# Kernel optimization log

Measured on AMD Instinct MI355X. Metric: run time of the kernel, lower is better.

The kernel has to match this reference:

```python
import jax, jax.numpy as jnp
import numpy as np

K = 1024          # codebook size
D = 64            # embedding dim
CC = 0.25         # commitment cost


def setup_inputs() -> dict:
    key = jax.random.key(0)
    k1, k2 = jax.random.split(key)
    inputs = jax.random.normal(k1, (64, 64, 32, 32), dtype=jnp.float32)  # [B, C=D, H, W]
    # nn.Embedding weight init: uniform(-1/K, 1/K)
    embedding = jax.random.uniform(k2, (K, D), dtype=jnp.float32,
                                   minval=-1.0 / K, maxval=1.0 / K)
    return {"inputs": inputs, "embedding": embedding}


def reference(inputs, embedding):
    # NCHW -> NHWC
    x = jnp.transpose(inputs, (0, 2, 3, 1))            # [B, H, W, D]
    B, H, W, Dd = x.shape
    flat = x.reshape(-1, Dd)                           # [N, D]
    distances = (jnp.sum(flat * flat, axis=1, keepdims=True)
                 - 2.0 * flat @ embedding.T
                 + jnp.sum(embedding * embedding, axis=1)[None, :])
    encoding_indices = jnp.argmin(distances, axis=1)   # [N]
    encodings = encoding_indices.reshape(B, H, W)      # [B, H, W]
    quantized = embedding[encodings]                   # [B, H, W, D]

    e_latent_loss = jnp.mean((jax.lax.stop_gradient(quantized) - x) ** 2)
    q_latent_loss = jnp.mean((quantized - jax.lax.stop_gradient(x)) ** 2)
    loss = q_latent_loss + CC * e_latent_loss

    # straight-through estimator
    quantized_st = x + jax.lax.stop_gradient(quantized - x)
    out = jnp.transpose(quantized_st, (0, 3, 1, 2))    # NHWC -> NCHW
    nll = jnp.ones((1,), dtype=jnp.float32)
    return out, encodings, loss, nll
```

## Files before the change

### kernel.cpp

```cpp
#include <hip/hip_runtime.h>
#include <stdint.h>

constexpr int KCODES = 1024;
constexpr int DDIM   = 64;
constexpr int HW     = 1024;
constexpr int NPTS   = 65536;
constexpr int PPB    = 64;
constexpr int NBLK   = NPTS / PPB;

constexpr int OUT_Q    = 0;
constexpr int OUT_IDX  = 4194304;
constexpr int OUT_LOSS = 4259840;
constexpr int OUT_NLL  = 4259841;

constexpr int WS_MAXC  = 0;
constexpr int WS_C     = 16;
constexpr int WS_E     = 2048;
constexpr int WS_PART  = 34816;

typedef __attribute__((ext_vector_type(8))) short short8v;
typedef __attribute__((ext_vector_type(4))) float float4v;

__device__ __forceinline__ uint16_t f2bf(float f) {
    uint32_t u = __float_as_uint(f);
    return (uint16_t)((u + 0x7fffu + ((u >> 16) & 1u)) >> 16);
}
__device__ __forceinline__ uint32_t pack2bf(float a, float b) {
    return (uint32_t)f2bf(a) | ((uint32_t)f2bf(b) << 16);
}

__device__ __forceinline__ float np_pairwise_sumsq64(const float* a) {
    float r[8];
    #pragma unroll
    for (int j = 0; j < 8; ++j) r[j] = __fmul_rn(a[j], a[j]);
    #pragma unroll
    for (int i = 8; i < 64; i += 8)
        #pragma unroll
        for (int j = 0; j < 8; ++j)
            r[j] = __fadd_rn(r[j], __fmul_rn(a[i + j], a[i + j]));
    return __fadd_rn(__fadd_rn(__fadd_rn(r[0], r[1]), __fadd_rn(r[2], r[3])),
                     __fadd_rn(__fadd_rn(r[4], r[5]), __fadd_rn(r[6], r[7])));
}

__global__ __launch_bounds__(256) void vq_init(const float* __restrict__ emb,
                                               float* __restrict__ ws) {
    __shared__ float smax[4];
    const int k = blockIdx.x * 256 + threadIdx.x;
    float row[DDIM];
    const float4* src = (const float4*)(emb + (size_t)k * DDIM);
    #pragma unroll
    for (int j = 0; j < 16; ++j) ((float4*)row)[j] = src[j];
    float C = np_pairwise_sumsq64(row);
    ws[WS_C + k] = C;
    {
        const int c = k >> 4, col = k & 15;
        uint32_t* eb = (uint32_t*)ws + WS_E + c * 512;
        #pragma unroll
        for (int q = 0; q < 4; ++q) {
            uint32_t* d0 = eb + (q * 16 + col) * 4;
            uint32_t* d1 = eb + 256 + (q * 16 + col) * 4;
            #pragma unroll
            for (int j = 0; j < 4; ++j) {
                d0[j] = pack2bf(row[q * 8 + 2 * j],      row[q * 8 + 2 * j + 1]);
                d1[j] = pack2bf(row[32 + q * 8 + 2 * j], row[32 + q * 8 + 2 * j + 1]);
            }
        }
    }
    float m = C;
    #pragma unroll
    for (int off = 32; off > 0; off >>= 1) m = fmaxf(m, __shfl_down(m, off, 64));
    if ((threadIdx.x & 63) == 0) smax[threadIdx.x >> 6] = m;
    __syncthreads();
    if (threadIdx.x == 0)
        ws[WS_MAXC + blockIdx.x] =
            fmaxf(fmaxf(smax[0], smax[1]), fmaxf(smax[2], smax[3]));
}

__global__ __launch_bounds__(256, 4) void vq_main(
        const float* __restrict__ inp, const float* __restrict__ emb,
        float* __restrict__ ws, float* __restrict__ out)
{
    __shared__ float    sAp[PPB][4];
    __shared__ float    sA[PPB];
    __shared__ float    sPart[4][PPB];
    __shared__ float    sThr[PPB];
    __shared__ uint16_t sCand[PPB * 4 * 8];
    __shared__ uint8_t  sCnt[PPB * 4];
    __shared__ int      sWin[PPB];
    __shared__ float    sred[4];

    const int tid  = threadIdx.x;
    const int lane = tid & 63;
    const int wave = tid >> 6;
    const int col  = lane & 15;
    const int quad = lane >> 4;
    const int base = blockIdx.x * PPB;
    const int b    = base >> 10;
    const int hw0  = base & 1023;

    {
        const int pp = tid >> 2;
        const int jj = (tid & 3) * 2;
        const float* xin = inp + (size_t)b * DDIM * HW + (hw0 + pp);
        float r0, r1;
        {
            float v0 = xin[(size_t)jj * HW];
            float v1 = xin[(size_t)(jj + 1) * HW];
            r0 = __fmul_rn(v0, v0);
            r1 = __fmul_rn(v1, v1);
        }
        #pragma unroll
        for (int i = 8; i < 64; i += 8) {
            float v0 = xin[(size_t)(i + jj) * HW];
            float v1 = xin[(size_t)(i + jj + 1) * HW];
            r0 = __fadd_rn(r0, __fmul_rn(v0, v0));
            r1 = __fadd_rn(r1, __fmul_rn(v1, v1));
        }
        sAp[pp][tid & 3] = __fadd_rn(r0, r1);
    }

    short8v a[4][2];
    #pragma unroll
    for (int g = 0; g < 4; ++g) {
        const float* xp = inp + (size_t)b * DDIM * HW + (hw0 + g * 16 + col);
        short8v t0, t1;
        #pragma unroll
        for (int j = 0; j < 8; ++j) {
            t0[j] = (short)f2bf(xp[(size_t)(quad * 8 + j) * HW]);
            t1[j] = (short)f2bf(xp[(size_t)(32 + quad * 8 + j) * HW]);
        }
        a[g][0] = t0; a[g][1] = t1;
    }

    const char* Eb = (const char*)((const uint32_t*)ws + WS_E);
    const char* Ew = Eb + (size_t)wave * 16 * 2048 + (size_t)lane * 16;
    const float* Cw = ws + WS_C;
    const int k0 = wave * 256;

    float smaxv[4][4];
    #pragma unroll
    for (int g = 0; g < 4; ++g)
        #pragma unroll
        for (int r = 0; r < 4; ++r) smaxv[g][r] = -3.0e38f;

    {
        short8v pa0 = *(const short8v*)(Ew);
        short8v pa1 = *(const short8v*)(Ew + 1024);
        short8v pb0 = *(const short8v*)(Ew + 2048);
        short8v pb1 = *(const short8v*)(Ew + 2048 + 1024);
        float   cia = Cw[k0 + col] * -0.5f;
        float   cib = Cw[k0 + 16 + col] * -0.5f;
        #pragma unroll 1
        for (int c2 = 0; c2 < 16; c2 += 2) {
            short8v u0 = pa0, u1 = pa1; float uci = cia;
            if (c2 + 2 < 16) {
                const char* er = Ew + (size_t)(c2 + 2) * 2048;
                pa0 = *(const short8v*)(er);
                pa1 = *(const short8v*)(er + 1024);
                cia = Cw[k0 + (c2 + 2) * 16 + col] * -0.5f;
            }
            float4v ci4 = {uci, uci, uci, uci};
            #pragma unroll
            for (int g = 0; g < 4; ++g) {
                float4v acc = ci4;
                acc = __builtin_amdgcn_mfma_f32_16x16x32_bf16(a[g][0], u0, acc, 0, 0, 0);
                acc = __builtin_amdgcn_mfma_f32_16x16x32_bf16(a[g][1], u1, acc, 0, 0, 0);
                #pragma unroll
                for (int r = 0; r < 4; ++r) smaxv[g][r] = fmaxf(smaxv[g][r], acc[r]);
            }
            short8v v0 = pb0, v1 = pb1; float vci = cib;
            if (c2 + 3 < 16) {
                const char* er = Ew + (size_t)(c2 + 3) * 2048;
                pb0 = *(const short8v*)(er);
                pb1 = *(const short8v*)(er + 1024);
                cib = Cw[k0 + (c2 + 3) * 16 + col] * -0.5f;
            }
            float4v ci4b = {vci, vci, vci, vci};
            #pragma unroll
            for (int g = 0; g < 4; ++g) {
                float4v acc = ci4b;
                acc = __builtin_amdgcn_mfma_f32_16x16x32_bf16(a[g][0], v0, acc, 0, 0, 0);
                acc = __builtin_amdgcn_mfma_f32_16x16x32_bf16(a[g][1], v1, acc, 0, 0, 0);
                #pragma unroll
                for (int r = 0; r < 4; ++r) smaxv[g][r] = fmaxf(smaxv[g][r], acc[r]);
            }
        }
    }
    #pragma unroll
    for (int g = 0; g < 4; ++g)
        #pragma unroll
        for (int r = 0; r < 4; ++r) {
            float m = smaxv[g][r];
            m = fmaxf(m, __shfl_xor(m, 1, 16));
            m = fmaxf(m, __shfl_xor(m, 2, 16));
            m = fmaxf(m, __shfl_xor(m, 4, 16));
            m = fmaxf(m, __shfl_xor(m, 8, 16));
            if (col == 0) sPart[wave][g * 16 + quad * 4 + r] = m;
        }
    __syncthreads();

    if (tid < PPB) {
        float A = __fadd_rn(__fadd_rn(sAp[tid][0], sAp[tid][1]),
                            __fadd_rn(sAp[tid][2], sAp[tid][3]));
        sA[tid] = A;
        float gm = fmaxf(fmaxf(sPart[0][tid], sPart[1][tid]),
                         fmaxf(sPart[2][tid], sPart[3][tid]));
        float mc = fmaxf(fmaxf(ws[WS_MAXC], ws[WS_MAXC + 1]),
                         fmaxf(ws[WS_MAXC + 2], ws[WS_MAXC + 3]));
        sThr[tid] = gm - (0.015625f * sqrtf(A) * sqrtf(mc) + 6e-5f);
    }
    __syncthreads();

    float thr[4][4];
    #pragma unroll
    for (int g = 0; g < 4; ++g)
        #pragma unroll
        for (int r = 0; r < 4; ++r) thr[g][r] = sThr[g * 16 + quad * 4 + r];

    int cnt[4][4];
    #pragma unroll
    for (int g = 0; g < 4; ++g)
        #pragma unroll
        for (int r = 0; r < 4; ++r) cnt[g][r] = 0;

    {
        short8v pa0 = *(const short8v*)(Ew);
        short8v pa1 = *(const short8v*)(Ew + 1024);
        short8v pb0 = *(const short8v*)(Ew + 2048);
        short8v pb1 = *(const short8v*)(Ew + 2048 + 1024);
        float   cia = Cw[k0 + col] * -0.5f;
        float   cib = Cw[k0 + 16 + col] * -0.5f;
        #pragma unroll 1
        for (int c2 = 0; c2 < 16; c2 += 2) {
            short8v u0 = pa0, u1 = pa1; float uci = cia;
            if (c2 + 2 < 16) {
                const char* er = Ew + (size_t)(c2 + 2) * 2048;
                pa0 = *(const short8v*)(er);
                pa1 = *(const short8v*)(er + 1024);
                cia = Cw[k0 + (c2 + 2) * 16 + col] * -0.5f;
            }
            float4v ci4 = {uci, uci, uci, uci};
            #pragma unroll
            for (int g = 0; g < 4; ++g) {
                float4v acc = ci4;
                acc = __builtin_amdgcn_mfma_f32_16x16x32_bf16(a[g][0], u0, acc, 0, 0, 0);
                acc = __builtin_amdgcn_mfma_f32_16x16x32_bf16(a[g][1], u1, acc, 0, 0, 0);
                #pragma unroll
                for (int r = 0; r < 4; ++r) {
                    unsigned long long bm = __ballot(acc[r] >= thr[g][r]);
                    if (col == 0) {
                        unsigned gm = (unsigned)(bm >> (quad * 16)) & 0xffffu;
                        while (gm) {
                            int bit = __ffs(gm) - 1;
                            gm &= gm - 1;
                            int ct = cnt[g][r];
                            if (ct < 8)
                                sCand[((g * 16 + quad * 4 + r) * 4 + wave) * 8 + ct] =
                                    (uint16_t)(k0 + c2 * 16 + bit);
                            cnt[g][r] = ct + 1;
                        }
                    }
                }
            }
            short8v v0 = pb0, v1 = pb1; float vci = cib;
            if (c2 + 3 < 16) {
                const char* er = Ew + (size_t)(c2 + 3) * 2048;
                pb0 = *(const short8v*)(er);
                pb1 = *(const short8v*)(er + 1024);
                cib = Cw[k0 + (c2 + 3) * 16 + col] * -0.5f;
            }
            float4v ci4b = {vci, vci, vci, vci};
            #pragma unroll
            for (int g = 0; g < 4; ++g) {
                float4v acc = ci4b;
                acc = __builtin_amdgcn_mfma_f32_16x16x32_bf16(a[g][0], v0, acc, 0, 0, 0);
                acc = __builtin_amdgcn_mfma_f32_16x16x32_bf16(a[g][1], v1, acc, 0, 0, 0);
                #pragma unroll
                for (int r = 0; r < 4; ++r) {
                    unsigned long long bm = __ballot(acc[r] >= thr[g][r]);
                    if (col == 0) {
                        unsigned gm = (unsigned)(bm >> (quad * 16)) & 0xffffu;
                        while (gm) {
                            int bit = __ffs(gm) - 1;
                            gm &= gm - 1;
                            int ct = cnt[g][r];
                            if (ct < 8)
                                sCand[((g * 16 + quad * 4 + r) * 4 + wave) * 8 + ct] =
                                    (uint16_t)(k0 + (c2 + 1) * 16 + bit);
                            cnt[g][r] = ct + 1;
                        }
                    }
                }
            }
        }
    }
    if (col == 0) {
        #pragma unroll
        for (int g = 0; g < 4; ++g)
            #pragma unroll
            for (int r = 0; r < 4; ++r) {
                int c = cnt[g][r];
                sCnt[(g * 16 + quad * 4 + r) * 4 + wave] = (uint8_t)(c > 255 ? 255 : c);
            }
    }
    __syncthreads();

    if (tid < PPB) {
        const int p = tid, n = base + p;
        int cq[4], tot = 0, cmax = 0;
        #pragma unroll
        for (int q = 0; q < 4; ++q) {
            cq[q] = sCnt[p * 4 + q];
            tot += cq[q];
            cmax = cq[q] > cmax ? cq[q] : cmax;
        }
        int win;
        if (tot == 1) {
            win = 0;
            #pragma unroll
            for (int q = 0; q < 4; ++q)
                if (cq[q]) win = sCand[(p * 4 + q) * 8];
        } else {
            const float* xin = inp + (size_t)b * DDIM * HW + (hw0 + p);
            float x[DDIM];
            #pragma unroll
            for (int d = 0; d < DDIM; ++d) x[d] = xin[(size_t)d * HW];
            const float A = sA[p];
            float bd = 3.0e38f; win = KCODES - 1;
            if (cmax <= 8) {
                #pragma unroll 1
                for (int q = 0; q < 4; ++q) {
                    #pragma unroll 1
                    for (int i = 0; i < cq[q]; ++i) {
                        int k = sCand[(p * 4 + q) * 8 + i];
                        float e[DDIM];
                        const float4* e4 = (const float4*)(emb + (size_t)k * DDIM);
                        #pragma unroll
                        for (int j = 0; j < 16; ++j) ((float4*)e)[j] = e4[j];
                        float g = 0.f;
                        #pragma unroll
                        for (int d = 0; d < DDIM; ++d) g = fmaf(x[d], e[d], g);
                        float dd = __fadd_rn(__fsub_rn(A, __fmul_rn(2.0f, g)), Cw[k]);
                        if (dd < bd || (dd == bd && k < win)) { bd = dd; win = k; }
                    }
                }
            } else {
                #pragma unroll 1
                for (int k = 0; k < KCODES; ++k) {
                    float e[DDIM];
                    const float4* e4 = (const float4*)(emb + (size_t)k * DDIM);
                    #pragma unroll
                    for (int j = 0; j < 16; ++j) ((float4*)e)[j] = e4[j];
                    float g = 0.f;
                    #pragma unroll
                    for (int d = 0; d < DDIM; ++d) g = fmaf(x[d], e[d], g);
                    float dd = __fadd_rn(__fsub_rn(A, __fmul_rn(2.0f, g)), Cw[k]);
                    if (dd < bd) { bd = dd; win = k; }
                }
            }
        }
        sWin[p] = win;
        out[OUT_IDX + n] = (float)win;
    }
    __syncthreads();

    {
        const int pl = tid & 63, qtr = tid >> 6;
        const int win = sWin[pl];
        const int ch0 = qtr * 16;
        float q[16];
        const float4* q4 = (const float4*)(emb + (size_t)win * DDIM + ch0);
        #pragma unroll
        for (int j = 0; j < 4; ++j) ((float4*)q)[j] = q4[j];
        const size_t off = (size_t)b * DDIM * HW + (size_t)ch0 * HW + (hw0 + pl);
        const float* xin2 = inp + off;
        float* orow = out + off;
        float lacc = 0.f;
        #pragma unroll
        for (int j = 0; j < 16; ++j) {
            float xv = xin2[(size_t)j * HW];
            float diff = __fsub_rn(q[j], xv);
            orow[(size_t)j * HW] = __fadd_rn(xv, diff);
            lacc = fmaf(diff, diff, lacc);
        }
        #pragma unroll
        for (int o2 = 32; o2 > 0; o2 >>= 1) lacc += __shfl_down(lacc, o2, 64);
        if (lane == 0) sred[wave] = lacc;
    }
    __syncthreads();
    if (tid == 0)
        ws[WS_PART + blockIdx.x] = sred[0] + sred[1] + sred[2] + sred[3];
}

__global__ __launch_bounds__(256) void vq_fin(const float* __restrict__ ws,
                                              float* __restrict__ out) {
    __shared__ float sred[4];
    const int tid = threadIdx.x;
    float s = 0.f;
    #pragma unroll
    for (int j = 0; j < 4; ++j) s += ws[WS_PART + j * 256 + tid];
    #pragma unroll
    for (int off = 32; off > 0; off >>= 1) s += __shfl_down(s, off, 64);
    if ((tid & 63) == 0) sred[tid >> 6] = s;
    __syncthreads();
    if (tid == 0) {
        float L = sred[0] + sred[1] + sred[2] + sred[3];
        out[OUT_LOSS] = L * (1.25f / 4194304.0f);
        out[OUT_NLL]  = 1.0f;
    }
}

extern "C" void kernel_launch(void* const* d_in, const int* in_sizes, int n_in,
                              void* d_out, int out_size, void* d_ws, size_t ws_size,
                              hipStream_t stream) {
    const float* inp = (const float*)d_in[0];
    const float* emb = (const float*)d_in[1];
    float* out = (float*)d_out;
    float* ws  = (float*)d_ws;

    vq_init<<<4, 256, 0, stream>>>(emb, ws);
    vq_main<<<NBLK, 256, 0, stream>>>(inp, emb, ws, out);
    vq_fin<<<1, 256, 0, stream>>>(ws, out);
}
```

Measured before the change: 119.8 us.

## Stage inputs in LDS, use 8 waves per block, fuse final loss reduction

Input tiles are loaded once with coalesced float4 reads into a padded LDS buffer. The MFMA A-fragments, squared norms, candidate rescoring and the output pass all read that buffer instead of issuing strided global loads. Blocks grow to 512 threads so each of 8 waves scans 128 codes. The separate finalize kernel is replaced by a last-block-done atomic counter, which removes one launch. The trade-offs are more LDS and register pressure per block and a serialized tail in the last block.

```diff
diff --git a/kernel.cpp b/kernel.cpp
--- a/kernel.cpp
+++ b/kernel.cpp
@@ -8,7 +8,6 @@
 constexpr int PPB    = 64;
 constexpr int NBLK   = NPTS / PPB;
 
-constexpr int OUT_Q    = 0;
 constexpr int OUT_IDX  = 4194304;
 constexpr int OUT_LOSS = 4259840;
 constexpr int OUT_NLL  = 4259841;
@@ -17,6 +16,9 @@
 constexpr int WS_C     = 16;
 constexpr int WS_E     = 2048;
 constexpr int WS_PART  = 34816;
+constexpr int WS_CTR   = 35840;
+
+constexpr int XS_STR = 65;
 
 typedef __attribute__((ext_vector_type(8))) short short8v;
 typedef __attribute__((ext_vector_type(4))) float float4v;
@@ -42,10 +44,9 @@
                      __fadd_rn(__fadd_rn(r[4], r[5]), __fadd_rn(r[6], r[7])));
 }
 
-__global__ __launch_bounds__(256) void vq_init(const float* __restrict__ emb,
-                                               float* __restrict__ ws) {
-    __shared__ float smax[4];
-    const int k = blockIdx.x * 256 + threadIdx.x;
+__global__ __launch_bounds__(64) void vq_init(const float* __restrict__ emb,
+                                              float* __restrict__ ws) {
+    const int k = blockIdx.x * 64 + threadIdx.x;
     float row[DDIM];
     const float4* src = (const float4*)(emb + (size_t)k * DDIM);
     #pragma unroll
@@ -69,25 +70,25 @@
     float m = C;
     #pragma unroll
     for (int off = 32; off > 0; off >>= 1) m = fmaxf(m, __shfl_down(m, off, 64));
-    if ((threadIdx.x & 63) == 0) smax[threadIdx.x >> 6] = m;
-    __syncthreads();
-    if (threadIdx.x == 0)
-        ws[WS_MAXC + blockIdx.x] =
-            fmaxf(fmaxf(smax[0], smax[1]), fmaxf(smax[2], smax[3]));
-}
-
-__global__ __launch_bounds__(256, 4) void vq_main(
+    if (threadIdx.x == 0) ws[WS_MAXC + blockIdx.x] = m;
+    if (k == 0) ((uint32_t*)ws)[WS_CTR] = 0u;
+}
+
+__global__ __launch_bounds__(512, 8) void vq_main(
         const float* __restrict__ inp, const float* __restrict__ emb,
         float* __restrict__ ws, float* __restrict__ out)
 {
-    __shared__ float    sAp[PPB][4];
+    __shared__ float    xs[DDIM * XS_STR];
+    __shared__ uint4    xb4[PPB * 8];
+    __shared__ float    sAp[PPB][8];
     __shared__ float    sA[PPB];
-    __shared__ float    sPart[4][PPB];
+    __shared__ float    sPart[8][PPB];
     __shared__ float    sThr[PPB];
-    __shared__ uint16_t sCand[PPB * 4 * 8];
-    __shared__ uint8_t  sCnt[PPB * 4];
+    __shared__ uint16_t sCand[PPB * 8 * 8];
+    __shared__ uint8_t  sCnt[PPB * 8];
     __shared__ int      sWin[PPB];
     __shared__ float    sred[4];
+    __shared__ int      sLast;
 
     const int tid  = threadIdx.x;
     const int lane = tid & 63;
@@ -98,44 +99,59 @@
     const int b    = base >> 10;
     const int hw0  = base & 1023;
 
-    {
-        const int pp = tid >> 2;
-        const int jj = (tid & 3) * 2;
-        const float* xin = inp + (size_t)b * DDIM * HW + (hw0 + pp);
-        float r0, r1;
-        {
-            float v0 = xin[(size_t)jj * HW];
-            float v1 = xin[(size_t)(jj + 1) * HW];
-            r0 = __fmul_rn(v0, v0);
-            r1 = __fmul_rn(v1, v1);
-        }
-        #pragma unroll
-        for (int i = 8; i < 64; i += 8) {
-            float v0 = xin[(size_t)(i + jj) * HW];
-            float v1 = xin[(size_t)(i + jj + 1) * HW];
-            r0 = __fadd_rn(r0, __fmul_rn(v0, v0));
-            r1 = __fadd_rn(r1, __fmul_rn(v1, v1));
-        }
-        sAp[pp][tid & 3] = __fadd_rn(r0, r1);
-    }
+    const float* xg = inp + (size_t)b * DDIM * HW + hw0;
+
+    {
+        const int f4 = tid & 15;
+        #pragma unroll
+        for (int it = 0; it < 2; ++it) {
+            const int d = (tid >> 4) + it * 32;
+            float4 v = *(const float4*)(xg + (size_t)d * HW + f4 * 4);
+            float* dst = &xs[d * XS_STR + f4 * 4];
+            dst[0] = v.x; dst[1] = v.y; dst[2] = v.z; dst[3] = v.w;
+        }
+    }
+    __syncthreads();
+
+    {
+        const int p = tid >> 3, seg = tid & 7;
+        uint32_t w0 = pack2bf(xs[(seg * 8 + 0) * XS_STR + p],
+                              xs[(seg * 8 + 1) * XS_STR + p]);
+        uint32_t w1 = pack2bf(xs[(seg * 8 + 2) * XS_STR + p],
+                              xs[(seg * 8 + 3) * XS_STR + p]);
+        uint32_t w2 = pack2bf(xs[(seg * 8 + 4) * XS_STR + p],
+                              xs[(seg * 8 + 5) * XS_STR + p]);
+        uint32_t w3 = pack2bf(xs[(seg * 8 + 6) * XS_STR + p],
+                              xs[(seg * 8 + 7) * XS_STR + p]);
+        xb4[p * 8 + (seg ^ (p & 7))] = make_uint4(w0, w1, w2, w3);
+
+        float v = xs[seg * XS_STR + p];
+        float r = __fmul_rn(v, v);
+        #pragma unroll
+        for (int i = 1; i < 8; ++i) {
+            float vv = xs[(8 * i + seg) * XS_STR + p];
+            r = __fadd_rn(r, __fmul_rn(vv, vv));
+        }
+        sAp[p][seg] = r;
+    }
+    __syncthreads();
 
     short8v a[4][2];
-    #pragma unroll
-    for (int g = 0; g < 4; ++g) {
-        const float* xp = inp + (size_t)b * DDIM * HW + (hw0 + g * 16 + col);
-        short8v t0, t1;
-        #pragma unroll
-        for (int j = 0; j < 8; ++j) {
-            t0[j] = (short)f2bf(xp[(size_t)(quad * 8 + j) * HW]);
-            t1[j] = (short)f2bf(xp[(size_t)(32 + quad * 8 + j) * HW]);
-        }
-        a[g][0] = t0; a[g][1] = t1;
+    {
+        const short8v* xbv = (const short8v*)xb4;
+        #pragma unroll
+        for (int g = 0; g < 4; ++g) {
+            const int row = g * 16 + col;
+            const int sw  = row & 7;
+            a[g][0] = xbv[row * 8 + ((0 + quad) ^ sw)];
+            a[g][1] = xbv[row * 8 + ((4 + quad) ^ sw)];
+        }
     }
 
     const char* Eb = (const char*)((const uint32_t*)ws + WS_E);
-    const char* Ew = Eb + (size_t)wave * 16 * 2048 + (size_t)lane * 16;
+    const char* Ew = Eb + (size_t)wave * 8 * 2048 + (size_t)lane * 16;
     const float* Cw = ws + WS_C;
-    const int k0 = wave * 256;
+    const int k0 = wave * 128;
 
     float smaxv[4][4];
     #pragma unroll
@@ -147,13 +163,13 @@
         short8v pa0 = *(const short8v*)(Ew);
         short8v pa1 = *(const short8v*)(Ew + 1024);
         short8v pb0 = *(const short8v*)(Ew + 2048);
-        short8v pb1 = *(const short8v*)(Ew + 2048 + 1024);
+        short8v pb1 = *(const short8v*)(Ew + 3072);
         float   cia = Cw[k0 + col] * -0.5f;
         float   cib = Cw[k0 + 16 + col] * -0.5f;
         #pragma unroll 1
-        for (int c2 = 0; c2 < 16; c2 += 2) {
+        for (int c2 = 0; c2 < 8; c2 += 2) {
             short8v u0 = pa0, u1 = pa1; float uci = cia;
-            if (c2 + 2 < 16) {
+            if (c2 + 2 < 8) {
                 const char* er = Ew + (size_t)(c2 + 2) * 2048;
                 pa0 = *(const short8v*)(er);
                 pa1 = *(const short8v*)(er + 1024);
@@ -169,7 +185,7 @@
                 for (int r = 0; r < 4; ++r) smaxv[g][r] = fmaxf(smaxv[g][r], acc[r]);
             }
             short8v v0 = pb0, v1 = pb1; float vci = cib;
-            if (c2 + 3 < 16) {
+            if (c2 + 3 < 8) {
                 const char* er = Ew + (size_t)(c2 + 3) * 2048;
                 pb0 = *(const short8v*)(er);
                 pb1 = *(const short8v*)(er + 1024);
@@ -200,13 +216,20 @@
     __syncthreads();
 
     if (tid < PPB) {
-        float A = __fadd_rn(__fadd_rn(sAp[tid][0], sAp[tid][1]),
-                            __fadd_rn(sAp[tid][2], sAp[tid][3]));
+        float A = __fadd_rn(
+            __fadd_rn(__fadd_rn(sAp[tid][0], sAp[tid][1]),
+                      __fadd_rn(sAp[tid][2], sAp[tid][3])),
+            __fadd_rn(__fadd_rn(sAp[tid][4], sAp[tid][5]),
+                      __fadd_rn(sAp[tid][6], sAp[tid][7])));
         sA[tid] = A;
-        float gm = fmaxf(fmaxf(sPart[0][tid], sPart[1][tid]),
-                         fmaxf(sPart[2][tid], sPart[3][tid]));
-        float mc = fmaxf(fmaxf(ws[WS_MAXC], ws[WS_MAXC + 1]),
-                         fmaxf(ws[WS_MAXC + 2], ws[WS_MAXC + 3]));
+        float gm = fmaxf(
+            fmaxf(fmaxf(sPart[0][tid], sPart[1][tid]),
+                  fmaxf(sPart[2][tid], sPart[3][tid])),
+            fmaxf(fmaxf(sPart[4][tid], sPart[5][tid]),
+                  fmaxf(sPart[6][tid], sPart[7][tid])));
+        float mc = ws[WS_MAXC];
+        #pragma unroll
+        for (int j = 1; j < 16; ++j) mc = fmaxf(mc, ws[WS_MAXC + j]);
         sThr[tid] = gm - (0.015625f * sqrtf(A) * sqrtf(mc) + 6e-5f);
     }
     __syncthreads();
@@ -227,13 +250,13 @@
         short8v pa0 = *(const short8v*)(Ew);
         short8v pa1 = *(const short8v*)(Ew + 1024);
         short8v pb0 = *(const short8v*)(Ew + 2048);
-        short8v pb1 = *(const short8v*)(Ew + 2048 + 1024);
+        short8v pb1 = *(const short8v*)(Ew + 3072);
         float   cia = Cw[k0 + col] * -0.5f;
         float   cib = Cw[k0 + 16 + col] * -0.5f;
         #pragma unroll 1
-        for (int c2 = 0; c2 < 16; c2 += 2) {
+        for (int c2 = 0; c2 < 8; c2 += 2) {
             short8v u0 = pa0, u1 = pa1; float uci = cia;
-            if (c2 + 2 < 16) {
+            if (c2 + 2 < 8) {
                 const char* er = Ew + (size_t)(c2 + 2) * 2048;
                 pa0 = *(const short8v*)(er);
                 pa1 = *(const short8v*)(er + 1024);
@@ -255,7 +278,7 @@
                             gm &= gm - 1;
                             int ct = cnt[g][r];
                             if (ct < 8)
-                                sCand[((g * 16 + quad * 4 + r) * 4 + wave) * 8 + ct] =
+                                sCand[((g * 16 + quad * 4 + r) * 8 + wave) * 8 + ct] =
                                     (uint16_t)(k0 + c2 * 16 + bit);
                             cnt[g][r] = ct + 1;
                         }
@@ -263,7 +286,7 @@
                 }
             }
             short8v v0 = pb0, v1 = pb1; float vci = cib;
-            if (c2 + 3 < 16) {
+            if (c2 + 3 < 8) {
                 const char* er = Ew + (size_t)(c2 + 3) * 2048;
                 pb0 = *(const short8v*)(er);
                 pb1 = *(const short8v*)(er + 1024);
@@ -285,7 +308,7 @@
                             gm &= gm - 1;
                             int ct = cnt[g][r];
                             if (ct < 8)
-                                sCand[((g * 16 + quad * 4 + r) * 4 + wave) * 8 + ct] =
+                                sCand[((g * 16 + quad * 4 + r) * 8 + wave) * 8 + ct] =
                                     (uint16_t)(k0 + (c2 + 1) * 16 + bit);
                             cnt[g][r] = ct + 1;
                         }
@@ -300,46 +323,46 @@
             #pragma unroll
             for (int r = 0; r < 4; ++r) {
                 int c = cnt[g][r];
-                sCnt[(g * 16 + quad * 4 + r) * 4 + wave] = (uint8_t)(c > 255 ? 255 : c);
+                sCnt[(g * 16 + quad * 4 + r) * 8 + wave] = (uint8_t)(c > 255 ? 255 : c);
             }
     }
     __syncthreads();
 
     if (tid < PPB) {
         const int p = tid, n = base + p;
-        int cq[4], tot = 0, cmax = 0;
-        #pragma unroll
-        for (int q = 0; q < 4; ++q) {
-            cq[q] = sCnt[p * 4 + q];
-            tot += cq[q];
-            cmax = cq[q] > cmax ? cq[q] : cmax;
+        int tot = 0, cmaxc = 0;
+        #pragma unroll
+        for (int wq = 0; wq < 8; ++wq) {
+            int c = sCnt[p * 8 + wq];
+            tot += c;
+            cmaxc = c > cmaxc ? c : cmaxc;
         }
         int win;
         if (tot == 1) {
             win = 0;
             #pragma unroll
-            for (int q = 0; q < 4; ++q)
-                if (cq[q]) win = sCand[(p * 4 + q) * 8];
+            for (int wq = 0; wq < 8; ++wq)
+                if (sCnt[p * 8 + wq]) win = sCand[(p * 8 + wq) * 8];
         } else {
-            const float* xin = inp + (size_t)b * DDIM * HW + (hw0 + p);
-            float x[DDIM];
-            #pragma unroll
-            for (int d = 0; d < DDIM; ++d) x[d] = xin[(size_t)d * HW];
             const float A = sA[p];
             float bd = 3.0e38f; win = KCODES - 1;
-            if (cmax <= 8) {
+            if (cmaxc <= 8) {
                 #pragma unroll 1
-                for (int q = 0; q < 4; ++q) {
+                for (int wq = 0; wq < 8; ++wq) {
+                    int c = sCnt[p * 8 + wq];
                     #pragma unroll 1
-                    for (int i = 0; i < cq[q]; ++i) {
-                        int k = sCand[(p * 4 + q) * 8 + i];
-                        float e[DDIM];
+                    for (int i = 0; i < c; ++i) {
+                        int k = sCand[(p * 8 + wq) * 8 + i];
                         const float4* e4 = (const float4*)(emb + (size_t)k * DDIM);
-                        #pragma unroll
-                        for (int j = 0; j < 16; ++j) ((float4*)e)[j] = e4[j];
                         float g = 0.f;
                         #pragma unroll
-                        for (int d = 0; d < DDIM; ++d) g = fmaf(x[d], e[d], g);
+                        for (int j = 0; j < 16; ++j) {
+                            float4 ev = e4[j];
+                            g = fmaf(xs[(4 * j + 0) * XS_STR + p], ev.x, g);
+                            g = fmaf(xs[(4 * j + 1) * XS_STR + p], ev.y, g);
+                            g = fmaf(xs[(4 * j + 2) * XS_STR + p], ev.z, g);
+                            g = fmaf(xs[(4 * j + 3) * XS_STR + p], ev.w, g);
+                        }
                         float dd = __fadd_rn(__fsub_rn(A, __fmul_rn(2.0f, g)), Cw[k]);
                         if (dd < bd || (dd == bd && k < win)) { bd = dd; win = k; }
                     }
@@ -347,13 +370,16 @@
             } else {
                 #pragma unroll 1
                 for (int k = 0; k < KCODES; ++k) {
-                    float e[DDIM];
                     const float4* e4 = (const float4*)(emb + (size_t)k * DDIM);
-                    #pragma unroll
-                    for (int j = 0; j < 16; ++j) ((float4*)e)[j] = e4[j];
                     float g = 0.f;
                     #pragma unroll
-                    for (int d = 0; d < DDIM; ++d) g = fmaf(x[d], e[d], g);
+                    for (int j = 0; j < 16; ++j) {
+                        float4 ev = e4[j];
+                        g = fmaf(xs[(4 * j + 0) * XS_STR + p], ev.x, g);
+                        g = fmaf(xs[(4 * j + 1) * XS_STR + p], ev.y, g);
+                        g = fmaf(xs[(4 * j + 2) * XS_STR + p], ev.z, g);
+                        g = fmaf(xs[(4 * j + 3) * XS_STR + p], ev.w, g);
+                    }
                     float dd = __fadd_rn(__fsub_rn(A, __fmul_rn(2.0f, g)), Cw[k]);
                     if (dd < bd) { bd = dd; win = k; }
                 }
@@ -364,7 +390,7 @@
     }
     __syncthreads();
 
-    {
+    if (tid < 256) {
         const int pl = tid & 63, qtr = tid >> 6;
         const int win = sWin[pl];
         const int ch0 = qtr * 16;
@@ -373,40 +399,44 @@
         #pragma unroll
         for (int j = 0; j < 4; ++j) ((float4*)q)[j] = q4[j];
         const size_t off = (size_t)b * DDIM * HW + (size_t)ch0 * HW + (hw0 + pl);
-        const float* xin2 = inp + off;
         float* orow = out + off;
         float lacc = 0.f;
         #pragma unroll
         for (int j = 0; j < 16; ++j) {
-            float xv = xin2[(size_t)j * HW];
+            float xv = xs[(ch0 + j) * XS_STR + pl];
             float diff = __fsub_rn(q[j], xv);
             orow[(size_t)j * HW] = __fadd_rn(xv, diff);
             lacc = fmaf(diff, diff, lacc);
         }
         #pragma unroll
         for (int o2 = 32; o2 > 0; o2 >>= 1) lacc += __shfl_down(lacc, o2, 64);
-        if (lane == 0) sred[wave] = lacc;
-    }
-    __syncthreads();
-    if (tid == 0)
+        if (lane == 0) sred[qtr] = lacc;
+    }
+    __syncthreads();
+
+    if (tid == 0) {
         ws[WS_PART + blockIdx.x] = sred[0] + sred[1] + sred[2] + sred[3];
-}
-
-__global__ __launch_bounds__(256) void vq_fin(const float* __restrict__ ws,
-                                              float* __restrict__ out) {
-    __shared__ float sred[4];
-    const int tid = threadIdx.x;
-    float s = 0.f;
-    #pragma unroll
-    for (int j = 0; j < 4; ++j) s += ws[WS_PART + j * 256 + tid];
-    #pragma unroll
-    for (int off = 32; off > 0; off >>= 1) s += __shfl_down(s, off, 64);
-    if ((tid & 63) == 0) sred[tid >> 6] = s;
-    __syncthreads();
-    if (tid == 0) {
-        float L = sred[0] + sred[1] + sred[2] + sred[3];
-        out[OUT_LOSS] = L * (1.25f / 4194304.0f);
-        out[OUT_NLL]  = 1.0f;
+        __threadfence();
+        unsigned int old = atomicAdd((unsigned int*)ws + WS_CTR, 1u);
+        sLast = (old == NBLK - 1) ? 1 : 0;
+    }
+    __syncthreads();
+    if (sLast) {
+        __threadfence();
+        if (tid < 256) {
+            float s = 0.f;
+            #pragma unroll
+            for (int j = 0; j < 4; ++j) s += ws[WS_PART + j * 256 + tid];
+            #pragma unroll
+            for (int off = 32; off > 0; off >>= 1) s += __shfl_down(s, off, 64);
+            if ((tid & 63) == 0) sred[tid >> 6] = s;
+        }
+        __syncthreads();
+        if (tid == 0) {
+            float L = sred[0] + sred[1] + sred[2] + sred[3];
+            out[OUT_LOSS] = L * (1.25f / 4194304.0f);
+            out[OUT_NLL]  = 1.0f;
+        }
     }
 }
 
@@ -418,7 +448,6 @@
     float* out = (float*)d_out;
     float* ws  = (float*)d_ws;
 
-    vq_init<<<4, 256, 0, stream>>>(emb, ws);
-    vq_main<<<NBLK, 256, 0, stream>>>(inp, emb, ws, out);
-    vq_fin<<<1, 256, 0, stream>>>(ws, out);
-}
+    vq_init<<<16, 64, 0, stream>>>(emb, ws);
+    vq_main<<<NBLK, 512, 0, stream>>>(inp, emb, ws, out);
+}
```

After: 378.0 us. 3.15x slower.
